# Performance work log

Hardware: AMD Instinct MI355X
Metric: run time of the kernel (lower is better)

## Reference

```python
import jax, jax.numpy as jnp
import numpy as np

N, U, K, S = 1024, 64, 2, 2        # nodes, rnn_units, max_diffusion_step, num_supports
Q = S * K + 1                       # diffusion matrices (incl. identity)
B, T, H = 64, 12, 12                # batch, seq_len, horizon
IN, OUT, L = 1, 1, 2                # input_dim, output_dim, num_rnn_layers


def setup_inputs() -> dict:
    key = jax.random.key(0)
    ks = jax.random.split(key, 16)

    def glorot(k, shape):
        fan = shape[0] + shape[-1]
        return jax.random.normal(k, shape, jnp.float32) * np.float32(np.sqrt(2.0 / fan))

    # random-walk supports from a random dense adjacency (DCRNN: transpose of D^-1 A)
    adj = jax.random.uniform(ks[0], (N, N), jnp.float32)
    rw = lambda a: a / a.sum(axis=1, keepdims=True)
    supports = jnp.stack([rw(adj).T, rw(adj.T).T])  # (S, N, N)

    inputs = jax.random.normal(ks[1], (B, N * IN, T), jnp.float32)

    p = {}
    i = 2
    for pre, ind in (("enc", IN), ("dec", OUT)):
        for l in range(L):
            f = (ind if l == 0 else U) + U
            p[f"{pre}_gw{l}"] = glorot(ks[i], (Q * f, 2 * U)); i += 1
            p[f"{pre}_gb{l}"] = jnp.ones((2 * U,), jnp.float32)   # GRU gate bias init 1.0
            p[f"{pre}_cw{l}"] = glorot(ks[i], (Q * f, U)); i += 1
            p[f"{pre}_cb{l}"] = jnp.zeros((U,), jnp.float32)
    p["proj_w"] = glorot(ks[i], (U, OUT))
    p["proj_b"] = jnp.zeros((OUT,), jnp.float32)
    return {"inputs": inputs, "supports": supports, **p}


def _diffusion(x, supports):
    # x: (B, N, F) -> (B, N, Q*F); Chebyshev-style recurrence as in DCGRUCell._gconv
    mats = [x]
    for s in range(S):
        A = supports[s]
        x0 = x
        x1 = jnp.einsum('nm,bmf->bnf', A, x0)
        mats.append(x1)
        for _ in range(2, K + 1):
            x2 = 2.0 * jnp.einsum('nm,bmf->bnf', A, x1) - x0
            mats.append(x2)
            x0, x1 = x1, x2
    return jnp.concatenate(mats, axis=-1)


def _cell(x, h, supports, gw, gb, cw, cb):
    # x: (B,N,Fin), h: (B,N,U)
    ru = jax.nn.sigmoid(_diffusion(jnp.concatenate([x, h], -1), supports) @ gw + gb)
    r, u = ru[..., :U], ru[..., U:]
    c = jnp.tanh(_diffusion(jnp.concatenate([x, r * h], -1), supports) @ cw + cb)
    return u * h + (1.0 - u) * c


def reference(inputs, supports,
              enc_gw0, enc_gb0, enc_cw0, enc_cb0,
              enc_gw1, enc_gb1, enc_cw1, enc_cb1,
              dec_gw0, dec_gb0, dec_cw0, dec_cb0,
              dec_gw1, dec_gb1, dec_cw1, dec_cb1,
              proj_w, proj_b):
    enc = [(enc_gw0, enc_gb0, enc_cw0, enc_cb0), (enc_gw1, enc_gb1, enc_cw1, enc_cb1)]
    dec = [(dec_gw0, dec_gb0, dec_cw0, dec_cb0), (dec_gw1, dec_gb1, dec_cw1, dec_cb1)]

    x_seq = inputs.reshape(B, N, IN, T).transpose(3, 0, 1, 2)  # (T, B, N, IN)
    h0 = jnp.zeros((L, B, N, U), inputs.dtype)

    def enc_step(h, x):
        out, hs = x, []
        for l in range(L):
            hn = _cell(out, h[l], supports, *enc[l])
            hs.append(hn)
            out = hn
        return jnp.stack(hs), None

    hT, _ = jax.lax.scan(enc_step, h0, x_seq)

    def dec_step(carry, _):
        h, xin = carry
        out, hs = xin, []
        for l in range(L):
            hn = _cell(out, h[l], supports, *dec[l])
            hs.append(hn)
            out = hn
        proj = out @ proj_w + proj_b          # (B, N, OUT)
        return (jnp.stack(hs), proj), proj.reshape(B, N * OUT)

    go = jnp.zeros((B, N, OUT), inputs.dtype)
    _, outs = jax.lax.scan(dec_step, (hT, go), None, length=H)
    return outs  # (H, B, N*OUT)
```

## Files before the change

kernel.cpp:

```cpp
#include <hip/hip_runtime.h>

typedef _Float16 f16;
typedef _Float16 f16x4 __attribute__((ext_vector_type(4)));
typedef _Float16 f16x8 __attribute__((ext_vector_type(8)));
typedef float    f32x4 __attribute__((ext_vector_type(4)));

#define NN 1024
#define NB 64
#define NT 12
#define NHOR 12
#define ROWS (NN*NB)
static const long SLOT = (long)ROWS*64;

#define LDA_S 40
#define LDZ_S 136

struct DiffP {
  const f16* A;
  const f16* z1; long ldz1; int nct1; f16* o1; long ldo1;
  const f16* z2; long ldz2; int nct2; f16* o2; long ldo2; int cv2;
  int K; int matsq;
};

__global__ __launch_bounds__(256) void gemm_diff(DiffP p) {
  __shared__ f16 As[128*LDA_S];
  __shared__ f16 Zs[32*LDZ_S];
  const int rt = blockIdx.x, ct = blockIdx.y;
  const f16* zptr; long ldz; f16* optr; long ldo; int cvalid; long c0;
  if (ct < p.nct1) { c0=(long)ct*128; zptr=p.z1; ldz=p.ldz1; optr=p.o1; ldo=p.ldo1; cvalid=128; }
  else { c0=(long)(ct-p.nct1)*128; zptr=p.z2; ldz=p.ldz2; optr=p.o2; ldo=p.ldo2; cvalid=p.cv2; }
  const int tid=threadIdx.x, lane=tid&63, wv=tid>>6;
  const int wm=(wv>>1)*64, wc=(wv&1)*64;
  const int rq=lane>>4, ro=lane&15, lk=rq*4;
  f32x4 acc[4][4] = {};
  const long r0 = (long)rt*128;
  for (int k0=0; k0<p.K; k0+=32) {
    #pragma unroll
    for (int it=0; it<2; ++it) {
      const int t = tid + it*256;
      const int m = t>>2, sg = t&3;
      f16x8 v = *(const f16x8*)(p.A + (r0+m)*1024 + k0 + sg*8);
      *(f16x8*)(&As[m*LDA_S + sg*8]) = v;
    }
    #pragma unroll
    for (int it=0; it<2; ++it) {
      const int t = tid + it*256;
      const int kz = t>>4, c8 = t&15;
      if (c8*8 < cvalid) {
        f16x8 v = *(const f16x8*)(zptr + (long)(k0+kz)*ldz + c0 + c8*8);
        *(f16x8*)(&Zs[kz*LDZ_S + c8*8]) = v;
      }
    }
    __syncthreads();
    f16x8 a[4], b[4];
    #pragma unroll
    for (int i=0;i<4;i++) {
      const f16* ar = &As[(wm + i*16 + ro)*LDA_S + lk];
      f16x4 lo = *(const f16x4*)ar;
      f16x4 hi = *(const f16x4*)(ar + 16);
      f16x8 t2; t2[0]=lo[0];t2[1]=lo[1];t2[2]=lo[2];t2[3]=lo[3];
      t2[4]=hi[0];t2[5]=hi[1];t2[6]=hi[2];t2[7]=hi[3];
      a[i]=t2;
    }
    #pragma unroll
    for (int j=0;j<4;j++) {
      const int c = wc + j*16 + ro;
      f16x8 t2;
      #pragma unroll
      for (int jj=0;jj<4;jj++) t2[jj]   = Zs[(lk+jj)*LDZ_S + c];
      #pragma unroll
      for (int jj=0;jj<4;jj++) t2[4+jj] = Zs[(16+lk+jj)*LDZ_S + c];
      b[j]=t2;
    }
    #pragma unroll
    for (int i=0;i<4;i++)
      #pragma unroll
      for (int j=0;j<4;j++)
        acc[i][j] = __builtin_amdgcn_mfma_f32_16x16x32_f16(a[i], b[j], acc[i][j], 0,0,0);
    __syncthreads();
  }
  #pragma unroll
  for (int i=0;i<4;i++) {
    #pragma unroll
    for (int j=0;j<4;j++) {
      const int col = wc + j*16 + ro;
      if (col >= cvalid) continue;
      const long cg = c0 + col;
      #pragma unroll
      for (int e=0;e<4;e++) {
        const long rg = r0 + wm + i*16 + rq*4 + e;
        float v = acc[i][j][e];
        if (p.matsq) v = 2.f*v - ((rg==cg)?1.f:0.f);
        optr[rg*ldo + cg] = (f16)v;
      }
    }
  }
}

struct Tab5 { const f16* p[5]; };
struct CellP {
  Tab5 ta, tb, xq;
  const f16 *wa, *wb, *wx0;
  const float* bias;
  const float* h32in;
  f16* rh; float* u32;
  float* h32io; f16* h16io;
  int nseg, xf1;
};

template<int O, int GATE>
__global__ __launch_bounds__(256) void cell_gemm(CellP p) {
  constexpr int FC = O/32;
  constexpr int C8 = O/8;
  __shared__ f16 As[128*LDA_S];
  __shared__ f16 Zs[32*LDZ_S];
  const int tid=threadIdx.x, lane=tid&63, wv=tid>>6;
  const int wm=(wv>>1)*64, wc=(wv&1)*(O/2);
  const int rq=lane>>4, ro=lane&15, lk=rq*4;
  f32x4 acc[4][FC] = {};
  const long r0 = (long)blockIdx.x*128;
  const int Ktot = p.nseg*320;
  for (int kg=0; kg<Ktot; kg+=32) {
    const int seg = (kg>=320)?1:0;
    const int kk  = kg - seg*320;
    const int q = kk>>6, kq = kk&63;
    const f16* asrc = seg ? p.tb.p[q] : p.ta.p[q];
    const f16* wsrc = (seg ? p.wb : p.wa) + (long)kk*O;
    #pragma unroll
    for (int it=0; it<2; ++it) {
      const int t = tid + it*256;
      const int m = t>>2, sg = t&3;
      f16x8 v = *(const f16x8*)(asrc + (r0+m)*64 + kq + sg*8);
      *(f16x8*)(&As[m*LDA_S + sg*8]) = v;
    }
    #pragma unroll
    for (int it=0; it<(32*C8)/256; ++it) {
      const int t = tid + it*256;
      const int kz = t/C8, c8 = t%C8;
      f16x8 v = *(const f16x8*)(wsrc + (long)kz*O + c8*8);
      *(f16x8*)(&Zs[kz*LDZ_S + c8*8]) = v;
    }
    __syncthreads();
    f16x8 a[4], b[FC];
    #pragma unroll
    for (int i=0;i<4;i++) {
      const f16* ar = &As[(wm + i*16 + ro)*LDA_S + lk];
      f16x4 lo = *(const f16x4*)ar;
      f16x4 hi = *(const f16x4*)(ar + 16);
      f16x8 t2; t2[0]=lo[0];t2[1]=lo[1];t2[2]=lo[2];t2[3]=lo[3];
      t2[4]=hi[0];t2[5]=hi[1];t2[6]=hi[2];t2[7]=hi[3];
      a[i]=t2;
    }
    #pragma unroll
    for (int j=0;j<FC;j++) {
      const int c = wc + j*16 + ro;
      f16x8 t2;
      #pragma unroll
      for (int jj=0;jj<4;jj++) t2[jj]   = Zs[(lk+jj)*LDZ_S + c];
      #pragma unroll
      for (int jj=0;jj<4;jj++) t2[4+jj] = Zs[(16+lk+jj)*LDZ_S + c];
      b[j]=t2;
    }
    #pragma unroll
    for (int i=0;i<4;i++)
      #pragma unroll
      for (int j=0;j<FC;j++)
        acc[i][j] = __builtin_amdgcn_mfma_f32_16x16x32_f16(a[i], b[j], acc[i][j], 0,0,0);
    __syncthreads();
  }
  #pragma unroll
  for (int i=0;i<4;i++) {
    #pragma unroll
    for (int e=0;e<4;e++) {
      const long rg = r0 + wm + i*16 + rq*4 + e;
      float xv[5];
      if (p.xf1) {
        #pragma unroll
        for (int q2=0;q2<5;q2++) xv[q2] = (float)p.xq.p[q2][rg];
      }
      #pragma unroll
      for (int j=0;j<FC;j++) {
        const int col = wc + j*16 + ro;
        float v = acc[i][j][e] + p.bias[col];
        if (p.xf1) {
          #pragma unroll
          for (int q2=0;q2<5;q2++) v += xv[q2] * (float)p.wx0[q2*O + col];
        }
        if (GATE) {
          const float s = 1.f/(1.f + __expf(-v));
          if (col < 64) p.rh[rg*64 + col] = (f16)(s * p.h32in[rg*64 + col]);
          else          p.u32[rg*64 + (col-64)] = s;
        } else {
          const float cc = tanhf(v);
          const float u  = p.u32[rg*64 + col];
          const float h  = p.h32io[rg*64 + col];
          const float hn = u*h + (1.f-u)*cc;
          p.h32io[rg*64 + col] = hn;
          p.h16io[rg*64 + col] = (f16)hn;
        }
      }
    }
  }
}

__global__ void k_cast_sup(const float* s, f16* W) {
  long i = (long)blockIdx.x*256 + threadIdx.x;
  if (i >= 2LL*NN*NN) return;
  long ss = (i >= (long)NN*NN) ? 1 : 0;
  long off = i - ss*(long)NN*NN;
  W[ss*2*(long)NN*NN + off] = (f16)s[i];
}

__global__ void k_pack_x(const float* in, f16* xe) {
  int i = blockIdx.x*256 + threadIdx.x;
  if (i >= NT*ROWS) return;
  int t = i / ROWS, r = i % ROWS, n = r>>6, b = r&63;
  xe[i] = (f16)in[(long)b*NN*NT + (long)n*NT + t];
}

__global__ void k_split_w(const float* src, f16* dsth, f16* dstx, int f, int xf, int O) {
  int i = blockIdx.x*256 + threadIdx.x;
  if (i >= 5*f*O) return;
  int o = i % O, rr = i / O, q = rr / f, ff = rr % f;
  f16 v = (f16)src[i];
  if (ff < xf) dstx[(q*xf + ff)*O + o] = v;
  else         dsth[(q*64 + ff - xf)*O + o] = v;
}

__global__ void k_proj(const float* h32, const float* pw, const float* pb,
                       float* out, f16* xdec) {
  int r = blockIdx.x*256 + threadIdx.x;
  if (r >= ROWS) return;
  float acc = pb[0];
  const float* hp = h32 + (long)r*64;
  #pragma unroll
  for (int k=0;k<64;k++) acc += hp[k]*pw[k];
  int n = r>>6, b = r&63;
  out[(long)b*NN + n] = acc;
  xdec[r] = (f16)acc;
}

extern "C" void kernel_launch(void* const* d_in, const int* in_sizes, int n_in,
                              void* d_out, int out_size, void* d_ws, size_t ws_size,
                              hipStream_t stream) {
  (void)in_sizes; (void)n_in; (void)out_size; (void)ws_size;
  const float* inputs = (const float*)d_in[0];
  const float* sup    = (const float*)d_in[1];
  const float* gwp[4] = {(const float*)d_in[2], (const float*)d_in[6], (const float*)d_in[10], (const float*)d_in[14]};
  const float* gbp[4] = {(const float*)d_in[3], (const float*)d_in[7], (const float*)d_in[11], (const float*)d_in[15]};
  const float* cwp[4] = {(const float*)d_in[4], (const float*)d_in[8], (const float*)d_in[12], (const float*)d_in[16]};
  const float* cbp[4] = {(const float*)d_in[5], (const float*)d_in[9], (const float*)d_in[13], (const float*)d_in[17]};
  const float* pw = (const float*)d_in[18];
  const float* pb = (const float*)d_in[19];
  float* out = (float*)d_out;

  char* base = (char*)d_ws; size_t off = 0;
  auto alloc = [&](size_t bytes)->void* { void* p = base + off; off += (bytes + 255) & ~(size_t)255; return p; };
  f16* W16   = (f16*)alloc(4LL*NN*NN*2);
  f16* xenc  = (f16*)alloc((long)NT*ROWS*2);
  f16* xdec  = (f16*)alloc((long)ROWS*2);
  f16*  h16[2] = {(f16*)alloc(SLOT*2),  (f16*)alloc(SLOT*2)};
  float* h32[2] = {(float*)alloc(SLOT*4), (float*)alloc(SLOT*4)};
  float* u32 = (float*)alloc(SLOT*4);
  f16* rh    = (f16*)alloc(SLOT*2);
  f16* Dh    = (f16*)alloc(4*SLOT*2);
  f16* Dx    = (f16*)alloc(4*SLOT*2);
  f16* Dx0   = (f16*)alloc(4LL*ROWS*2);
  f16 *gwh[4], *gwx[4], *cwh[4], *cwx[4];
  for (int i=0;i<4;i++) {
    gwh[i]=(f16*)alloc(5*64*128*2); gwx[i]=(f16*)alloc(5*64*128*2);
    cwh[i]=(f16*)alloc(5*64*64*2);  cwx[i]=(f16*)alloc(5*64*64*2);
  }

  hipMemsetAsync(h16[0], 0, SLOT*2, stream);
  hipMemsetAsync(h16[1], 0, SLOT*2, stream);
  hipMemsetAsync(h32[0], 0, SLOT*4, stream);
  hipMemsetAsync(h32[1], 0, SLOT*4, stream);
  hipMemsetAsync(xdec,   0, (long)ROWS*2, stream);

  k_cast_sup<<<(2*NN*NN+255)/256, 256, 0, stream>>>(sup, W16);
  for (int s=0;s<2;s++) {
    DiffP mp{};
    mp.A = W16 + (long)s*2*NN*NN;
    mp.z1 = mp.A; mp.ldz1 = 1024; mp.nct1 = 8;
    mp.o1 = W16 + ((long)s*2+1)*NN*NN; mp.ldo1 = 1024;
    mp.nct2 = 0; mp.K = 1024; mp.matsq = 1;
    gemm_diff<<<dim3(8,8),256,0,stream>>>(mp);
  }
  k_pack_x<<<(NT*ROWS+255)/256,256,0,stream>>>(inputs, xenc);
  const int fs[4]  = {65,128,65,128};
  const int xfs[4] = {1,64,1,64};
  for (int i=0;i<4;i++) {
    k_split_w<<<(5*fs[i]*128+255)/256,256,0,stream>>>(gwp[i], gwh[i], gwx[i], fs[i], xfs[i], 128);
    k_split_w<<<(5*fs[i]*64 +255)/256,256,0,stream>>>(cwp[i], cwh[i], cwx[i], fs[i], xfs[i], 64);
  }

  auto run_cell = [&](const f16* x16, int xf, f16* h16c, float* h32c, int wi) {
    DiffP dp{};
    dp.A = W16; dp.K = 1024; dp.matsq = 0;
    dp.z1 = h16c; dp.ldz1 = 4096; dp.nct1 = 32; dp.o1 = Dh; dp.ldo1 = 4096;
    if (xf == 64) { dp.z2 = x16; dp.ldz2 = 4096; dp.nct2 = 32; dp.o2 = Dx;  dp.ldo2 = 4096; dp.cv2 = 128; }
    else          { dp.z2 = x16; dp.ldz2 = 64;   dp.nct2 = 1;  dp.o2 = Dx0; dp.ldo2 = 64;   dp.cv2 = 64;  }
    gemm_diff<<<dim3(32, dp.nct1 + dp.nct2), 256, 0, stream>>>(dp);
    CellP gp{};
    gp.ta.p[0] = h16c; for (int q=1;q<5;q++) gp.ta.p[q] = Dh + (long)(q-1)*SLOT;
    gp.wa = gwh[wi]; gp.bias = gbp[wi];
    gp.h32in = h32c; gp.rh = rh; gp.u32 = u32;
    if (xf == 64) {
      gp.nseg = 2; gp.xf1 = 0;
      gp.tb.p[0] = x16; for (int q=1;q<5;q++) gp.tb.p[q] = Dx + (long)(q-1)*SLOT;
      gp.wb = gwx[wi];
    } else {
      gp.nseg = 1; gp.xf1 = 1;
      gp.xq.p[0] = x16; for (int q=1;q<5;q++) gp.xq.p[q] = Dx0 + (long)(q-1)*ROWS;
      gp.wx0 = gwx[wi];
    }
    cell_gemm<128,1><<<512, 256, 0, stream>>>(gp);
    DiffP dp2{};
    dp2.A = W16; dp2.K = 1024; dp2.matsq = 0;
    dp2.z1 = rh; dp2.ldz1 = 4096; dp2.nct1 = 32; dp2.o1 = Dh; dp2.ldo1 = 4096;
    dp2.nct2 = 0;
    gemm_diff<<<dim3(32, 32), 256, 0, stream>>>(dp2);
    CellP cp{};
    cp.ta.p[0] = rh; for (int q=1;q<5;q++) cp.ta.p[q] = Dh + (long)(q-1)*SLOT;
    cp.wa = cwh[wi]; cp.bias = cbp[wi];
    cp.u32 = u32; cp.h32io = h32c; cp.h16io = h16c;
    if (xf == 64) {
      cp.nseg = 2; cp.xf1 = 0;
      cp.tb.p[0] = x16; for (int q=1;q<5;q++) cp.tb.p[q] = Dx + (long)(q-1)*SLOT;
      cp.wb = cwx[wi];
    } else {
      cp.nseg = 1; cp.xf1 = 1;
      cp.xq.p[0] = x16; for (int q=1;q<5;q++) cp.xq.p[q] = Dx0 + (long)(q-1)*ROWS;
      cp.wx0 = cwx[wi];
    }
    cell_gemm<64,0><<<512, 256, 0, stream>>>(cp);
  };

  for (int t=0;t<NT;t++) {
    run_cell(xenc + (long)t*ROWS, 1, h16[0], h32[0], 0);
    run_cell(h16[0],             64, h16[1], h32[1], 1);
  }
  for (int s=0;s<NHOR;s++) {
    run_cell(xdec,   1, h16[0], h32[0], 2);
    run_cell(h16[0], 64, h16[1], h32[1], 3);
    k_proj<<<ROWS/256, 256, 0, stream>>>(h32[1], pw, pb, out + (long)s*ROWS, xdec);
  }
}
```

Baseline: 12.46 ms.

## Transpose diffusion operands to K-contiguous layout with swizzled LDS and direct global-to-LDS loads

Both GEMM kernels now stage operands as K-contiguous rows through global_load_lds into XOR-swizzled shared memory, instead of strided per-element column reads. State and reset-gated state are transposed after each cell, and the weights and inputs are stored pre-transposed, so the diffusion GEMM reads both operands along K. Outputs are written as packed f16x4 vectors. The aim is to remove LDS bank conflicts and scalar B-fragment gathers, at the cost of extra transpose kernels and buffers each step.

```diff
diff --git a/kernel.cpp b/kernel.cpp
--- a/kernel.cpp
+++ b/kernel.cpp
@@ -6,72 +6,66 @@
 typedef float    f32x4 __attribute__((ext_vector_type(4)));
 
 #define NN 1024
-#define NB 64
 #define NT 12
 #define NHOR 12
-#define ROWS (NN*NB)
-static const long SLOT = (long)ROWS*64;
-
-#define LDA_S 40
-#define LDZ_S 136
+#define ROWS (NN*64)
+static const long SLOT = (long)NN*4096;
+
+__device__ __forceinline__ int swz(int row, int halfoff) {
+  return row*32 + ((((halfoff>>3) ^ row) & 3)<<3) + (halfoff&7);
+}
+
+template<int NR>
+__device__ __forceinline__ void stage_rows(f16* lds, const f16* src, long ldk, int k0, int w, int l) {
+  const int r4 = l>>2, c4 = l&3;
+  #pragma unroll
+  for (int ic=0; ic<NR/64; ++ic) {
+    const int row = (w + ic*4)*16 + r4;
+    const f16* g = src + (long)row*ldk + k0 + ((c4 ^ (row&3))<<3);
+    f16* d = lds + row*32 + c4*8;
+    __builtin_amdgcn_global_load_lds((const __attribute__((address_space(1))) void*)g,
+                                     (__attribute__((address_space(3))) void*)d, 16, 0, 0);
+  }
+}
+
+__device__ __forceinline__ f16x8 frag(const f16* lds, int row, int lk) {
+  f16x4 lo = *(const f16x4*)&lds[swz(row, lk)];
+  f16x4 hi = *(const f16x4*)&lds[swz(row, 16+lk)];
+  f16x8 r; r[0]=lo[0];r[1]=lo[1];r[2]=lo[2];r[3]=lo[3];
+  r[4]=hi[0];r[5]=hi[1];r[6]=hi[2];r[7]=hi[3];
+  return r;
+}
 
 struct DiffP {
-  const f16* A;
-  const f16* z1; long ldz1; int nct1; f16* o1; long ldo1;
-  const f16* z2; long ldz2; int nct2; f16* o2; long ldo2; int cv2;
-  int K; int matsq;
+  const f16* A0; const f16* A1; int nt0;
+  const f16* B;
+  f16* out0; f16* out1;
+  long ldo1;
+  int mode_x;
+  int wsq;
 };
 
 __global__ __launch_bounds__(256) void gemm_diff(DiffP p) {
-  __shared__ f16 As[128*LDA_S];
-  __shared__ f16 Zs[32*LDZ_S];
-  const int rt = blockIdx.x, ct = blockIdx.y;
-  const f16* zptr; long ldz; f16* optr; long ldo; int cvalid; long c0;
-  if (ct < p.nct1) { c0=(long)ct*128; zptr=p.z1; ldz=p.ldz1; optr=p.o1; ldo=p.ldo1; cvalid=128; }
-  else { c0=(long)(ct-p.nct1)*128; zptr=p.z2; ldz=p.ldz2; optr=p.o2; ldo=p.ldo2; cvalid=p.cv2; }
-  const int tid=threadIdx.x, lane=tid&63, wv=tid>>6;
-  const int wm=(wv>>1)*64, wc=(wv&1)*64;
-  const int rq=lane>>4, ro=lane&15, lk=rq*4;
+  __shared__ f16 As[128*32];
+  __shared__ f16 Bs[128*32];
+  const int tid=threadIdx.x, l=tid&63, w=tid>>6;
+  const int rq=l>>4, ro=l&15, lk=rq*4;
+  const int rt=blockIdx.x, ct=blockIdx.y;
+  const int part = (rt >= p.nt0);
+  const int rtl  = part ? (rt - p.nt0) : rt;
+  const f16* Abase = (part ? p.A1 : p.A0) + (long)rtl*128*1024;
+  const f16* Bbase = p.B + (long)ct*128*1024;
+  const int wm=(w>>1)*64, wc=(w&1)*64;
   f32x4 acc[4][4] = {};
-  const long r0 = (long)rt*128;
-  for (int k0=0; k0<p.K; k0+=32) {
-    #pragma unroll
-    for (int it=0; it<2; ++it) {
-      const int t = tid + it*256;
-      const int m = t>>2, sg = t&3;
-      f16x8 v = *(const f16x8*)(p.A + (r0+m)*1024 + k0 + sg*8);
-      *(f16x8*)(&As[m*LDA_S + sg*8]) = v;
-    }
-    #pragma unroll
-    for (int it=0; it<2; ++it) {
-      const int t = tid + it*256;
-      const int kz = t>>4, c8 = t&15;
-      if (c8*8 < cvalid) {
-        f16x8 v = *(const f16x8*)(zptr + (long)(k0+kz)*ldz + c0 + c8*8);
-        *(f16x8*)(&Zs[kz*LDZ_S + c8*8]) = v;
-      }
-    }
+  for (int k0=0; k0<1024; k0+=32) {
+    stage_rows<128>(As, Abase, 1024, k0, w, l);
+    stage_rows<128>(Bs, Bbase, 1024, k0, w, l);
     __syncthreads();
     f16x8 a[4], b[4];
     #pragma unroll
-    for (int i=0;i<4;i++) {
-      const f16* ar = &As[(wm + i*16 + ro)*LDA_S + lk];
-      f16x4 lo = *(const f16x4*)ar;
-      f16x4 hi = *(const f16x4*)(ar + 16);
-      f16x8 t2; t2[0]=lo[0];t2[1]=lo[1];t2[2]=lo[2];t2[3]=lo[3];
-      t2[4]=hi[0];t2[5]=hi[1];t2[6]=hi[2];t2[7]=hi[3];
-      a[i]=t2;
-    }
-    #pragma unroll
-    for (int j=0;j<4;j++) {
-      const int c = wc + j*16 + ro;
-      f16x8 t2;
-      #pragma unroll
-      for (int jj=0;jj<4;jj++) t2[jj]   = Zs[(lk+jj)*LDZ_S + c];
-      #pragma unroll
-      for (int jj=0;jj<4;jj++) t2[4+jj] = Zs[(16+lk+jj)*LDZ_S + c];
-      b[j]=t2;
-    }
+    for (int i=0;i<4;i++) a[i] = frag(As, wm + i*16 + ro, lk);
+    #pragma unroll
+    for (int j=0;j<4;j++) b[j] = frag(Bs, wc + j*16 + ro, lk);
     #pragma unroll
     for (int i=0;i<4;i++)
       #pragma unroll
@@ -79,20 +73,36 @@
         acc[i][j] = __builtin_amdgcn_mfma_f32_16x16x32_f16(a[i], b[j], acc[i][j], 0,0,0);
     __syncthreads();
   }
+  const int c0 = ct*128;
+  if (p.wsq) {
+    #pragma unroll
+    for (int i=0;i<4;i++)
+      #pragma unroll
+      for (int j=0;j<4;j++) {
+        const int cg = c0 + wc + j*16 + ro;
+        #pragma unroll
+        for (int e=0;e<4;e++) {
+          const long rg = (long)rt*128 + wm + i*16 + rq*4 + e;
+          float v = 2.f*acc[i][j][e] - ((rg==cg)?1.f:0.f);
+          p.out0[rg*p.ldo1 + cg] = (f16)v;
+        }
+      }
+    return;
+  }
+  f16* ob = part ? p.out1 : p.out0;
+  const int mode = part ? p.mode_x : 0;
   #pragma unroll
   for (int i=0;i<4;i++) {
+    const int crow = rtl*128 + wm + i*16 + rq*4;
     #pragma unroll
     for (int j=0;j<4;j++) {
-      const int col = wc + j*16 + ro;
-      if (col >= cvalid) continue;
-      const long cg = c0 + col;
-      #pragma unroll
-      for (int e=0;e<4;e++) {
-        const long rg = r0 + wm + i*16 + rq*4 + e;
-        float v = acc[i][j][e];
-        if (p.matsq) v = 2.f*v - ((rg==cg)?1.f:0.f);
-        optr[rg*ldo + cg] = (f16)v;
-      }
+      const int col = c0 + wc + j*16 + ro;
+      const int q = col>>10, n = col&1023;
+      f16x4 sv;
+      #pragma unroll
+      for (int e=0;e<4;e++) sv[e] = (f16)acc[i][j][e];
+      if (mode == 0)          *(f16x4*)(ob + (long)q*SLOT + (long)n*4096 + crow) = sv;
+      else if (crow < 64)     *(f16x4*)(ob + (long)q*ROWS + n*64 + crow) = sv;
     }
   }
 }
@@ -111,56 +121,28 @@
 template<int O, int GATE>
 __global__ __launch_bounds__(256) void cell_gemm(CellP p) {
   constexpr int FC = O/32;
-  constexpr int C8 = O/8;
-  __shared__ f16 As[128*LDA_S];
-  __shared__ f16 Zs[32*LDZ_S];
-  const int tid=threadIdx.x, lane=tid&63, wv=tid>>6;
-  const int wm=(wv>>1)*64, wc=(wv&1)*(O/2);
-  const int rq=lane>>4, ro=lane&15, lk=rq*4;
+  __shared__ f16 As[128*32];
+  __shared__ f16 Bs[O*32];
+  const int tid=threadIdx.x, l=tid&63, w=tid>>6;
+  const int rq=l>>4, ro=l&15, lk=rq*4;
+  const int wm=(w>>1)*64, wc=(w&1)*(O/2);
   f32x4 acc[4][FC] = {};
   const long r0 = (long)blockIdx.x*128;
   const int Ktot = p.nseg*320;
   for (int kg=0; kg<Ktot; kg+=32) {
-    const int seg = (kg>=320)?1:0;
+    const int seg = (kg>=320) ? 1 : 0;
     const int kk  = kg - seg*320;
     const int q = kk>>6, kq = kk&63;
-    const f16* asrc = seg ? p.tb.p[q] : p.ta.p[q];
-    const f16* wsrc = (seg ? p.wb : p.wa) + (long)kk*O;
-    #pragma unroll
-    for (int it=0; it<2; ++it) {
-      const int t = tid + it*256;
-      const int m = t>>2, sg = t&3;
-      f16x8 v = *(const f16x8*)(asrc + (r0+m)*64 + kq + sg*8);
-      *(f16x8*)(&As[m*LDA_S + sg*8]) = v;
-    }
-    #pragma unroll
-    for (int it=0; it<(32*C8)/256; ++it) {
-      const int t = tid + it*256;
-      const int kz = t/C8, c8 = t%C8;
-      f16x8 v = *(const f16x8*)(wsrc + (long)kz*O + c8*8);
-      *(f16x8*)(&Zs[kz*LDZ_S + c8*8]) = v;
-    }
+    const f16* asrc = (seg ? p.tb.p[q] : p.ta.p[q]) + r0*64;
+    const f16* wsrc = seg ? p.wb : p.wa;
+    stage_rows<128>(As, asrc, 64, kq, w, l);
+    stage_rows<O>(Bs, wsrc, 320, kk, w, l);
     __syncthreads();
     f16x8 a[4], b[FC];
     #pragma unroll
-    for (int i=0;i<4;i++) {
-      const f16* ar = &As[(wm + i*16 + ro)*LDA_S + lk];
-      f16x4 lo = *(const f16x4*)ar;
-      f16x4 hi = *(const f16x4*)(ar + 16);
-      f16x8 t2; t2[0]=lo[0];t2[1]=lo[1];t2[2]=lo[2];t2[3]=lo[3];
-      t2[4]=hi[0];t2[5]=hi[1];t2[6]=hi[2];t2[7]=hi[3];
-      a[i]=t2;
-    }
-    #pragma unroll
-    for (int j=0;j<FC;j++) {
-      const int c = wc + j*16 + ro;
-      f16x8 t2;
-      #pragma unroll
-      for (int jj=0;jj<4;jj++) t2[jj]   = Zs[(lk+jj)*LDZ_S + c];
-      #pragma unroll
-      for (int jj=0;jj<4;jj++) t2[4+jj] = Zs[(16+lk+jj)*LDZ_S + c];
-      b[j]=t2;
-    }
+    for (int i=0;i<4;i++) a[i] = frag(As, wm + i*16 + ro, lk);
+    #pragma unroll
+    for (int j=0;j<FC;j++) b[j] = frag(Bs, wc + j*16 + ro, lk);
     #pragma unroll
     for (int i=0;i<4;i++)
       #pragma unroll
@@ -203,6 +185,27 @@
   }
 }
 
+__global__ __launch_bounds__(256) void k_transpose(const f16* in, f16* out, int R, int C) {
+  __shared__ f16 T[64*66];
+  const long rb = (long)blockIdx.x*64, cb = (long)blockIdx.y*64;
+  const int t = threadIdx.x;
+  #pragma unroll
+  for (int it=0; it<2; ++it) {
+    const int r = (t>>3) + it*32, c8 = (t&7)*8;
+    f16x8 v = *(const f16x8*)(in + (rb+r)*C + cb + c8);
+    *(f16x8*)&T[r*66 + c8] = v;
+  }
+  __syncthreads();
+  #pragma unroll
+  for (int it=0; it<2; ++it) {
+    const int c = (t>>3) + it*32, r8 = (t&7)*8;
+    f16x8 v;
+    #pragma unroll
+    for (int j=0;j<8;j++) v[j] = T[(r8+j)*66 + c];
+    *(f16x8*)(out + (cb+c)*R + rb + r8) = v;
+  }
+}
+
 __global__ void k_cast_sup(const float* s, f16* W) {
   long i = (long)blockIdx.x*256 + threadIdx.x;
   if (i >= 2LL*NN*NN) return;
@@ -211,24 +214,30 @@
   W[ss*2*(long)NN*NN + off] = (f16)s[i];
 }
 
-__global__ void k_pack_x(const float* in, f16* xe) {
+__global__ void k_pack_x(const float* in, f16* xe, f16* xet) {
   int i = blockIdx.x*256 + threadIdx.x;
   if (i >= NT*ROWS) return;
   int t = i / ROWS, r = i % ROWS, n = r>>6, b = r&63;
-  xe[i] = (f16)in[(long)b*NN*NT + (long)n*NT + t];
-}
-
-__global__ void k_split_w(const float* src, f16* dsth, f16* dstx, int f, int xf, int O) {
+  float v = in[(long)b*NN*NT + (long)n*NT + t];
+  xe[i] = (f16)v;
+  xet[(long)t*128*1024 + (long)b*1024 + n] = (f16)v;
+}
+
+__global__ void k_split_w_t(const float* src, f16* wh_t, f16* wxA, int f, int xf, int O) {
   int i = blockIdx.x*256 + threadIdx.x;
   if (i >= 5*f*O) return;
   int o = i % O, rr = i / O, q = rr / f, ff = rr % f;
   f16 v = (f16)src[i];
-  if (ff < xf) dstx[(q*xf + ff)*O + o] = v;
-  else         dsth[(q*64 + ff - xf)*O + o] = v;
+  if (ff < xf) {
+    if (xf == 1) wxA[q*O + o] = v;
+    else         wxA[(long)o*320 + q*64 + ff] = v;
+  } else {
+    wh_t[(long)o*320 + q*64 + (ff - xf)] = v;
+  }
 }
 
 __global__ void k_proj(const float* h32, const float* pw, const float* pb,
-                       float* out, f16* xdec) {
+                       float* out, f16* xdec, f16* xdect) {
   int r = blockIdx.x*256 + threadIdx.x;
   if (r >= ROWS) return;
   float acc = pb[0];
@@ -238,6 +247,7 @@
   int n = r>>6, b = r&63;
   out[(long)b*NN + n] = acc;
   xdec[r] = (f16)acc;
+  xdect[(long)b*1024 + n] = (f16)acc;
 }
 
 extern "C" void kernel_launch(void* const* d_in, const int* in_sizes, int n_in,
@@ -256,70 +266,79 @@
 
   char* base = (char*)d_ws; size_t off = 0;
   auto alloc = [&](size_t bytes)->void* { void* p = base + off; off += (bytes + 255) & ~(size_t)255; return p; };
-  f16* W16   = (f16*)alloc(4LL*NN*NN*2);
-  f16* xenc  = (f16*)alloc((long)NT*ROWS*2);
-  f16* xdec  = (f16*)alloc((long)ROWS*2);
-  f16*  h16[2] = {(f16*)alloc(SLOT*2),  (f16*)alloc(SLOT*2)};
-  float* h32[2] = {(float*)alloc(SLOT*4), (float*)alloc(SLOT*4)};
-  float* u32 = (float*)alloc(SLOT*4);
-  f16* rh    = (f16*)alloc(SLOT*2);
+  f16* W16    = (f16*)alloc(4LL*NN*NN*2);
+  f16* xenc   = (f16*)alloc((long)NT*ROWS*2);
+  f16* xenct  = (f16*)alloc((long)NT*128*1024*2);
+  f16* xdec   = (f16*)alloc((long)ROWS*2);
+  f16* xdect  = (f16*)alloc(128L*1024*2);
+  f16*  h16[2]  = {(f16*)alloc((long)ROWS*64*2),  (f16*)alloc((long)ROWS*64*2)};
+  f16*  hhat[2] = {(f16*)alloc(4096L*1024*2),     (f16*)alloc(4096L*1024*2)};
+  float* h32[2] = {(float*)alloc((long)ROWS*64*4), (float*)alloc((long)ROWS*64*4)};
+  float* u32 = (float*)alloc((long)ROWS*64*4);
+  f16* rh    = (f16*)alloc((long)ROWS*64*2);
+  f16* rhhat = (f16*)alloc(4096L*1024*2);
   f16* Dh    = (f16*)alloc(4*SLOT*2);
   f16* Dx    = (f16*)alloc(4*SLOT*2);
   f16* Dx0   = (f16*)alloc(4LL*ROWS*2);
   f16 *gwh[4], *gwx[4], *cwh[4], *cwx[4];
   for (int i=0;i<4;i++) {
-    gwh[i]=(f16*)alloc(5*64*128*2); gwx[i]=(f16*)alloc(5*64*128*2);
-    cwh[i]=(f16*)alloc(5*64*64*2);  cwx[i]=(f16*)alloc(5*64*64*2);
-  }
-
-  hipMemsetAsync(h16[0], 0, SLOT*2, stream);
-  hipMemsetAsync(h16[1], 0, SLOT*2, stream);
-  hipMemsetAsync(h32[0], 0, SLOT*4, stream);
-  hipMemsetAsync(h32[1], 0, SLOT*4, stream);
+    gwh[i]=(f16*)alloc(128L*320*2); gwx[i]=(f16*)alloc(128L*320*2);
+    cwh[i]=(f16*)alloc(64L*320*2);  cwx[i]=(f16*)alloc(64L*320*2);
+  }
+
+  hipMemsetAsync(h16[0], 0, (long)ROWS*64*2, stream);
+  hipMemsetAsync(h16[1], 0, (long)ROWS*64*2, stream);
+  hipMemsetAsync(hhat[0], 0, 4096L*1024*2, stream);
+  hipMemsetAsync(hhat[1], 0, 4096L*1024*2, stream);
+  hipMemsetAsync(h32[0], 0, (long)ROWS*64*4, stream);
+  hipMemsetAsync(h32[1], 0, (long)ROWS*64*4, stream);
   hipMemsetAsync(xdec,   0, (long)ROWS*2, stream);
+  hipMemsetAsync(xdect,  0, 128L*1024*2, stream);
 
   k_cast_sup<<<(2*NN*NN+255)/256, 256, 0, stream>>>(sup, W16);
+  f16* At = Dh;
+  for (int s=0;s<2;s++)
+    k_transpose<<<dim3(16,16),256,0,stream>>>(W16 + (long)s*2*NN*NN, At + (long)s*NN*NN, 1024, 1024);
   for (int s=0;s<2;s++) {
     DiffP mp{};
-    mp.A = W16 + (long)s*2*NN*NN;
-    mp.z1 = mp.A; mp.ldz1 = 1024; mp.nct1 = 8;
-    mp.o1 = W16 + ((long)s*2+1)*NN*NN; mp.ldo1 = 1024;
-    mp.nct2 = 0; mp.K = 1024; mp.matsq = 1;
+    mp.A0 = W16 + (long)s*2*NN*NN; mp.A1 = mp.A0; mp.nt0 = 8;
+    mp.B  = At + (long)s*NN*NN;
+    mp.out0 = W16 + ((long)s*2+1)*NN*NN; mp.ldo1 = 1024; mp.wsq = 1;
     gemm_diff<<<dim3(8,8),256,0,stream>>>(mp);
   }
-  k_pack_x<<<(NT*ROWS+255)/256,256,0,stream>>>(inputs, xenc);
+  k_pack_x<<<(NT*ROWS+255)/256,256,0,stream>>>(inputs, xenc, xenct);
   const int fs[4]  = {65,128,65,128};
   const int xfs[4] = {1,64,1,64};
   for (int i=0;i<4;i++) {
-    k_split_w<<<(5*fs[i]*128+255)/256,256,0,stream>>>(gwp[i], gwh[i], gwx[i], fs[i], xfs[i], 128);
-    k_split_w<<<(5*fs[i]*64 +255)/256,256,0,stream>>>(cwp[i], cwh[i], cwx[i], fs[i], xfs[i], 64);
-  }
-
-  auto run_cell = [&](const f16* x16, int xf, f16* h16c, float* h32c, int wi) {
+    k_split_w_t<<<(5*fs[i]*128+255)/256,256,0,stream>>>(gwp[i], gwh[i], gwx[i], fs[i], xfs[i], 128);
+    k_split_w_t<<<(5*fs[i]*64 +255)/256,256,0,stream>>>(cwp[i], cwh[i], cwx[i], fs[i], xfs[i], 64);
+  }
+
+  auto run_cell = [&](const f16* xraw, const f16* xhat, int xf,
+                      f16* h16c, f16* hhatc, float* h32c, int wi) {
     DiffP dp{};
-    dp.A = W16; dp.K = 1024; dp.matsq = 0;
-    dp.z1 = h16c; dp.ldz1 = 4096; dp.nct1 = 32; dp.o1 = Dh; dp.ldo1 = 4096;
-    if (xf == 64) { dp.z2 = x16; dp.ldz2 = 4096; dp.nct2 = 32; dp.o2 = Dx;  dp.ldo2 = 4096; dp.cv2 = 128; }
-    else          { dp.z2 = x16; dp.ldz2 = 64;   dp.nct2 = 1;  dp.o2 = Dx0; dp.ldo2 = 64;   dp.cv2 = 64;  }
-    gemm_diff<<<dim3(32, dp.nct1 + dp.nct2), 256, 0, stream>>>(dp);
+    dp.A0 = hhatc; dp.nt0 = 32; dp.B = W16; dp.out0 = Dh;
+    int gx;
+    if (xf == 64) { dp.A1 = xhat; dp.out1 = Dx;  dp.mode_x = 0; gx = 64; }
+    else          { dp.A1 = xhat; dp.out1 = Dx0; dp.mode_x = 2; gx = 33; }
+    gemm_diff<<<dim3(gx, 32), 256, 0, stream>>>(dp);
     CellP gp{};
     gp.ta.p[0] = h16c; for (int q=1;q<5;q++) gp.ta.p[q] = Dh + (long)(q-1)*SLOT;
     gp.wa = gwh[wi]; gp.bias = gbp[wi];
     gp.h32in = h32c; gp.rh = rh; gp.u32 = u32;
     if (xf == 64) {
       gp.nseg = 2; gp.xf1 = 0;
-      gp.tb.p[0] = x16; for (int q=1;q<5;q++) gp.tb.p[q] = Dx + (long)(q-1)*SLOT;
+      gp.tb.p[0] = xraw; for (int q=1;q<5;q++) gp.tb.p[q] = Dx + (long)(q-1)*SLOT;
       gp.wb = gwx[wi];
     } else {
       gp.nseg = 1; gp.xf1 = 1;
-      gp.xq.p[0] = x16; for (int q=1;q<5;q++) gp.xq.p[q] = Dx0 + (long)(q-1)*ROWS;
+      gp.xq.p[0] = xraw; for (int q=1;q<5;q++) gp.xq.p[q] = Dx0 + (long)(q-1)*ROWS;
       gp.wx0 = gwx[wi];
     }
     cell_gemm<128,1><<<512, 256, 0, stream>>>(gp);
+    k_transpose<<<dim3(16,64),256,0,stream>>>(rh, rhhat, 1024, 4096);
     DiffP dp2{};
-    dp2.A = W16; dp2.K = 1024; dp2.matsq = 0;
-    dp2.z1 = rh; dp2.ldz1 = 4096; dp2.nct1 = 32; dp2.o1 = Dh; dp2.ldo1 = 4096;
-    dp2.nct2 = 0;
+    dp2.A0 = rhhat; dp2.A1 = rhhat; dp2.nt0 = 32; dp2.B = W16; dp2.out0 = Dh;
     gemm_diff<<<dim3(32, 32), 256, 0, stream>>>(dp2);
     CellP cp{};
     cp.ta.p[0] = rh; for (int q=1;q<5;q++) cp.ta.p[q] = Dh + (long)(q-1)*SLOT;
@@ -327,23 +346,24 @@
     cp.u32 = u32; cp.h32io = h32c; cp.h16io = h16c;
     if (xf == 64) {
       cp.nseg = 2; cp.xf1 = 0;
-      cp.tb.p[0] = x16; for (int q=1;q<5;q++) cp.tb.p[q] = Dx + (long)(q-1)*SLOT;
+      cp.tb.p[0] = xraw; for (int q=1;q<5;q++) cp.tb.p[q] = Dx + (long)(q-1)*SLOT;
       cp.wb = cwx[wi];
     } else {
       cp.nseg = 1; cp.xf1 = 1;
-      cp.xq.p[0] = x16; for (int q=1;q<5;q++) cp.xq.p[q] = Dx0 + (long)(q-1)*ROWS;
+      cp.xq.p[0] = xraw; for (int q=1;q<5;q++) cp.xq.p[q] = Dx0 + (long)(q-1)*ROWS;
       cp.wx0 = cwx[wi];
     }
     cell_gemm<64,0><<<512, 256, 0, stream>>>(cp);
+    k_transpose<<<dim3(16,64),256,0,stream>>>(h16c, hhatc, 1024, 4096);
   };
 
   for (int t=0;t<NT;t++) {
-    run_cell(xenc + (long)t*ROWS, 1, h16[0], h32[0], 0);
-    run_cell(h16[0],             64, h16[1], h32[1], 1);
+    run_cell(xenc + (long)t*ROWS, xenct + (long)t*128*1024, 1, h16[0], hhat[0], h32[0], 0);
+    run_cell(h16[0], hhat[0],                              64, h16[1], hhat[1], h32[1], 1);
   }
   for (int s=0;s<NHOR;s++) {
-    run_cell(xdec,   1, h16[0], h32[0], 2);
-    run_cell(h16[0], 64, h16[1], h32[1], 3);
-    k_proj<<<ROWS/256, 256, 0, stream>>>(h32[1], pw, pb, out + (long)s*ROWS, xdec);
-  }
-}
+    run_cell(xdec,   xdect,   1, h16[0], hhat[0], h32[0], 2);
+    run_cell(h16[0], hhat[0],64, h16[1], hhat[1], h32[1], 3);
+    k_proj<<<ROWS/256, 256, 0, stream>>>(h32[1], pw, pb, out + (long)s*ROWS, xdec, xdect);
+  }
+}
```

Measured after the change: 10.93 ms. -12.3%, faster.
